# Kernel optimization log

Hardware: AMD Instinct MI355X
Metric: run time of the kernel (lower is better)

## Reference

```python
import jax, jax.numpy as jnp
import numpy as np

N_NODES = 100000
N_REL = 4
N_EDGES = 400000
IN_F, H_F, OUT_F = 128, 128, 64


def setup_inputs() -> dict:
    key = jax.random.key(0)
    ks = jax.random.split(key, 7)
    x = jax.random.normal(ks[0], (N_NODES, IN_F), dtype=jnp.float32)
    src_idx = jax.random.randint(ks[1], (N_REL, N_EDGES), 0, N_NODES, dtype=jnp.int64)
    dst_idx = jax.random.randint(ks[2], (N_REL, N_EDGES), 0, N_NODES, dtype=jnp.int64)
    # Glorot-ish scale for the per-relation GraphConv weights
    W1 = jax.random.normal(ks[3], (N_REL, IN_F, H_F), dtype=jnp.float32) * (1.0 / np.sqrt(IN_F))
    b1 = jnp.zeros((N_REL, H_F), dtype=jnp.float32)
    W2 = jax.random.normal(ks[4], (N_REL, H_F, OUT_F), dtype=jnp.float32) * (1.0 / np.sqrt(H_F))
    b2 = jnp.zeros((N_REL, OUT_F), dtype=jnp.float32)
    return {"x": x, "src_idx": src_idx, "dst_idx": dst_idx,
            "W1": W1, "b1": b1, "W2": W2, "b2": b2}


def _graph_conv(x, src, dst, W, b):
    """DGL GraphConv with norm='both': out = D_in^{-1/2} A^T D_out^{-1/2} x W + b."""
    n = x.shape[0]
    ones = jnp.ones(src.shape[0], dtype=x.dtype)
    deg_out = jnp.maximum(jax.ops.segment_sum(ones, src, num_segments=n), 1.0)
    deg_in = jnp.maximum(jax.ops.segment_sum(ones, dst, num_segments=n), 1.0)
    xn = x * jax.lax.rsqrt(deg_out)[:, None]              # [N, F] src-side norm
    msg = jnp.take(xn, src, axis=0)                        # [E, F] gather
    agg = jax.ops.segment_sum(msg, dst, num_segments=n)   # [N, F] scatter-add
    agg = agg * jax.lax.rsqrt(deg_in)[:, None]            # dst-side norm
    return agg @ W + b


def _hetero_layer(x, src_idx, dst_idx, Ws, bs):
    # per-relation conv, sum-aggregated across relations (HeteroGraphConv 'sum')
    per_rel = jax.vmap(lambda s, d, W, b: _graph_conv(x, s, d, W, b))(src_idx, dst_idx, Ws, bs)
    return per_rel.sum(axis=0)


def reference(x, src_idx, dst_idx, W1, b1, W2, b2):
    h = jax.nn.relu(_hetero_layer(x, src_idx, dst_idx, W1, b1))
    return _hetero_layer(h, src_idx, dst_idx, W2, b2)
```

## Files before the change

### kernel.cpp

```cpp
#include <hip/hip_runtime.h>
#include <hip/hip_bf16.h>

#define NN 100000
#define NR 4
#define NE 400000
#define INF 128
#define HF 128
#define OUTF 64

#define WIN 16384
#define WIN2 (WIN / 2)
#define NWIN 7
#define SUB 16
#define SLICE (NE / SUB)

#define GB 782
#define CB 1563
#define CSRB (NR * CB)
#define PADB 391
#define FGRID (GB + CSRB + PADB)

typedef __attribute__((ext_vector_type(8))) short s16x8;
typedef __attribute__((ext_vector_type(4))) float f32x4;

__global__ __launch_bounds__(256) void deg_win_kernel(const int* __restrict__ src,
                                                      const int* __restrict__ dst,
                                                      unsigned int* __restrict__ parts) {
    __shared__ unsigned int hist[WIN2];
    int arr = blockIdx.z;
    int r   = blockIdx.y;
    int win = blockIdx.x / SUB;
    int sub = blockIdx.x % SUB;
    const int4* idx4 = (const int4*)((arr ? dst : src) + (size_t)r * NE + (size_t)sub * SLICE);
    int base = win * WIN;

    uint4 z4 = make_uint4(0, 0, 0, 0);
    for (int i = threadIdx.x; i < WIN2 / 4; i += 256) ((uint4*)hist)[i] = z4;
    __syncthreads();

    auto proc = [&](int4 v) {
        int a;
        a = v.x - base; if ((unsigned)a < WIN) atomicAdd(&hist[a >> 1], 1u << ((a & 1) << 4));
        a = v.y - base; if ((unsigned)a < WIN) atomicAdd(&hist[a >> 1], 1u << ((a & 1) << 4));
        a = v.z - base; if ((unsigned)a < WIN) atomicAdd(&hist[a >> 1], 1u << ((a & 1) << 4));
        a = v.w - base; if ((unsigned)a < WIN) atomicAdd(&hist[a >> 1], 1u << ((a & 1) << 4));
    };

    constexpr int NV = SLICE / 4;
    int i = threadIdx.x;
    for (; i + 256 < NV; i += 512) {
        int4 va = idx4[i];
        int4 vb = idx4[i + 256];
        proc(va);
        proc(vb);
    }
    if (i < NV) proc(idx4[i]);
    __syncthreads();

    unsigned int* outp = parts + ((((size_t)arr * NR + r) * NWIN + win) * SUB + sub) * WIN2;
    for (int j = threadIdx.x; j < WIN2 / 4; j += 256)
        ((uint4*)outp)[j] = ((const uint4*)hist)[j];
}

__global__ void red_norm_kernel(const unsigned int* __restrict__ parts, int* __restrict__ deg_tot,
                                float* __restrict__ rno, float* __restrict__ rni) {
    int n = blockIdx.x * blockDim.x + threadIdx.x;
    if (n >= NN) return;
    if (n == 0) deg_tot[NN] = 0;
    int win = n / WIN, off = n % WIN;
    int word = off >> 1, sh = (off & 1) << 4;
    int tot = 0;
    #pragma unroll
    for (int r = 0; r < NR; r++) {
        const unsigned int* p0 = parts + (((size_t)0 * NR + r) * NWIN + win) * SUB * WIN2 + word;
        const unsigned int* p1 = parts + (((size_t)1 * NR + r) * NWIN + win) * SUB * WIN2 + word;
        int so = 0, si = 0;
        #pragma unroll
        for (int s = 0; s < SUB; s++) {
            so += (p0[(size_t)s * WIN2] >> sh) & 0xFFFFu;
            si += (p1[(size_t)s * WIN2] >> sh) & 0xFFFFu;
        }
        rno[(size_t)r * NN + n] = rsqrtf(fmaxf((float)so, 1.0f));
        rni[(size_t)r * NN + n] = rsqrtf(fmaxf((float)si, 1.0f));
        tot += si;
    }
    deg_tot[n] = tot;
}

__global__ void scan_block_kernel(const int* __restrict__ in, int* __restrict__ out,
                                  int* __restrict__ blockSums, int n) {
    __shared__ int sd[256];
    int t = threadIdx.x;
    int base = blockIdx.x * 1024 + t * 4;
    int v[4];
    #pragma unroll
    for (int j = 0; j < 4; j++) v[j] = (base + j < n) ? ((in[base + j] + 7) & ~7) : 0;
    int ts = v[0] + v[1] + v[2] + v[3];
    sd[t] = ts;
    __syncthreads();
    int acc = ts;
    for (int off = 1; off < 256; off <<= 1) {
        int x = (t >= off) ? sd[t - off] : 0;
        __syncthreads();
        acc += x; sd[t] = acc;
        __syncthreads();
    }
    int run = acc - ts;
    #pragma unroll
    for (int j = 0; j < 4; j++) {
        if (base + j < n) out[base + j] = run;
        run += v[j];
    }
    if (t == 255) blockSums[blockIdx.x] = acc;
}

__global__ void scan_sums_kernel(int* __restrict__ blockSums, int nb) {
    __shared__ int sd[512];
    int t = threadIdx.x;
    int v = (t < nb) ? blockSums[t] : 0;
    sd[t] = v;
    __syncthreads();
    int acc = v;
    for (int off = 1; off < 512; off <<= 1) {
        int x = (t >= off) ? sd[t - off] : 0;
        __syncthreads();
        acc += x; sd[t] = acc;
        __syncthreads();
    }
    if (t < nb) blockSums[t] = acc - v;
}

__global__ void scan_add_kernel(int* __restrict__ row_ptr, const int* __restrict__ blockSums,
                                int* __restrict__ cursor, int n) {
    int i = blockIdx.x * blockDim.x + threadIdx.x;
    if (i < n) {
        int v = row_ptr[i] + blockSums[i >> 10];
        row_ptr[i] = v;
        if (i < NN) cursor[i] = v;
    }
}

__global__ void prep_kernel(const float* __restrict__ W1, const float* __restrict__ W2,
                            const float* __restrict__ b1, const float* __restrict__ b2,
                            __hip_bfloat16* __restrict__ Wt1, __hip_bfloat16* __restrict__ Wt2,
                            float* __restrict__ bsum1, float* __restrict__ bsum2) {
    if (blockIdx.x == 384) {
        int t = threadIdx.x;
        if (t < HF) {
            float s = 0.f;
            for (int r = 0; r < NR; r++) s += b1[r * HF + t];
            bsum1[t] = s;
        } else if (t < HF + OUTF) {
            int f = t - HF;
            float s = 0.f;
            for (int r = 0; r < NR; r++) s += b2[r * OUTF + f];
            bsum2[f] = s;
        }
        return;
    }
    int id = blockIdx.x * 256 + threadIdx.x;
    if (id < NR * HF * INF) {
        int r = id >> 14, rem = id & 16383;
        int n_ = rem >> 7, k = rem & 127;
        Wt1[id] = __float2bfloat16(W1[((size_t)r * INF + k) * HF + n_]);
    } else {
        int id2 = id - NR * HF * INF;
        if (id2 < NR * OUTF * HF) {
            int r = id2 >> 13, rem = id2 & 8191;
            int n_ = rem >> 7, k = rem & 127;
            Wt2[id2] = __float2bfloat16(W2[((size_t)r * HF + k) * OUTF + n_]);
        }
    }
}

__device__ __forceinline__ s16x8 pack_bf16x8(float4 a0, float4 a1) {
    union { s16x8 v; __hip_bfloat162 h[4]; } u;
    u.h[0] = __float22bfloat162_rn(make_float2(a0.x, a0.y));
    u.h[1] = __float22bfloat162_rn(make_float2(a0.z, a0.w));
    u.h[2] = __float22bfloat162_rn(make_float2(a1.x, a1.y));
    u.h[3] = __float22bfloat162_rn(make_float2(a1.z, a1.w));
    return u.v;
}

__device__ __forceinline__ void load_lds_16(const void* g, void* l) {
    __builtin_amdgcn_global_load_lds(
        (const __attribute__((address_space(1))) void*)g,
        (__attribute__((address_space(3))) void*)l, 16, 0, 0);
}

template<int F, typename AT>
__device__ __forceinline__ void gemm_body(int mbase, const AT* __restrict__ Xb,
                                          const __hip_bfloat16* __restrict__ Wt,
                                          __hip_bfloat16* __restrict__ Zb, int nrel,
                                          __hip_bfloat16* Bs) {
    constexpr int NT = F / 16;
    constexpr int NG = F * 16;

    int tid  = threadIdx.x;
    int wid  = tid >> 6;
    int lane = tid & 63;
    int quad = lane >> 4;
    int l16  = lane & 15;
    int sw   = l16 & 7;

    int bofs[4];
    #pragma unroll
    for (int kb = 0; kb < 4; kb++)
        bofs[kb] = l16 * 256 + (((kb * 4 + quad) ^ sw) << 4);

    s16x8 afr[2][4];
    #pragma unroll
    for (int mt = 0; mt < 2; mt++) {
        int mrow = mbase + mt * 64 + wid * 16 + l16;
        if (mrow >= NN) mrow = NN - 1;
        #pragma unroll
        for (int kb = 0; kb < 4; kb++) {
            if constexpr (sizeof(AT) == 4) {
                const float* xr = (const float*)Xb + (size_t)mrow * 128 + kb * 32 + quad * 8;
                float4 a0 = *(const float4*)xr;
                float4 a1 = *(const float4*)(xr + 4);
                afr[mt][kb] = pack_bf16x8(a0, a1);
            } else {
                afr[mt][kb] = *(const s16x8*)((const __hip_bfloat16*)Xb + (size_t)mrow * 128 + kb * 32 + quad * 8);
            }
        }
    }

    for (int rel = 0; rel < nrel; rel++) {
        if (rel) __syncthreads();

        {
            const char* W = (const char*)(Wt + (size_t)rel * F * 128);
            #pragma unroll
            for (int it = 0; it < NG / 256; it++) {
                int dg = it * 256 + tid;
                int sg = dg ^ ((dg >> 4) & 7);
                load_lds_16(W + (size_t)sg * 16, (char*)Bs + (size_t)(dg & ~63) * 16);
            }
        }
        __syncthreads();

        __hip_bfloat16* Z = Zb + (size_t)rel * NN * F;

        f32x4 acc[2][NT];
        #pragma unroll
        for (int nt = 0; nt < NT; nt++) {
            acc[0][nt] = (f32x4){0.f, 0.f, 0.f, 0.f};
            acc[1][nt] = (f32x4){0.f, 0.f, 0.f, 0.f};
            #pragma unroll
            for (int kb = 0; kb < 4; kb++) {
                s16x8 bfr = *(const s16x8*)((const char*)Bs + nt * 4096 + bofs[kb]);
                acc[0][nt] = __builtin_amdgcn_mfma_f32_16x16x32_bf16(bfr, afr[0][kb], acc[0][nt], 0, 0, 0);
                acc[1][nt] = __builtin_amdgcn_mfma_f32_16x16x32_bf16(bfr, afr[1][kb], acc[1][nt], 0, 0, 0);
            }
        }

        #pragma unroll
        for (int mt = 0; mt < 2; mt++) {
            int g = mbase + mt * 64 + wid * 16 + l16;
            if (g < NN) {
                #pragma unroll
                for (int nt = 0; nt < NT; nt++) {
                    union { uint2 u; __hip_bfloat162 h[2]; } o;
                    o.h[0] = __float22bfloat162_rn(make_float2(acc[mt][nt][0], acc[mt][nt][1]));
                    o.h[1] = __float22bfloat162_rn(make_float2(acc[mt][nt][2], acc[mt][nt][3]));
                    *(uint2*)(Z + (size_t)g * F + nt * 16 + quad * 4) = o.u;
                }
            }
        }
    }
}

__global__ __launch_bounds__(256, 3) void fused1_kernel(
        const float* __restrict__ x, const __hip_bfloat16* __restrict__ Wt1,
        __hip_bfloat16* __restrict__ Zb,
        const int* __restrict__ src, const int* __restrict__ dst,
        const float* __restrict__ rno, const float* __restrict__ rni,
        int* __restrict__ cursor, int2* __restrict__ edges,
        const int* __restrict__ row_ptr, const int* __restrict__ deg_tot) {
    __shared__ __attribute__((aligned(16))) __hip_bfloat16 Bs[HF * 128];
    int b = blockIdx.x;
    bool isg = (b % 3 == 1) && (b / 3 < GB);
    if (isg) {
        gemm_body<HF, float>((b / 3) * 128, x, Wt1, Zb, NR, Bs);
        return;
    }
    int cnt = (b <= 1) ? 0 : ((b + 1) / 3);
    if (cnt > GB) cnt = GB;
    int ng = b - cnt;
    if (ng < CSRB) {
        int r = ng / CB;
        int i = (ng % CB) * 256 + threadIdx.x;
        if (i < NE) {
            int s = src[(size_t)r * NE + i];
            int d = dst[(size_t)r * NE + i];
            int pos = atomicAdd(&cursor[d], 1);
            float c = rno[(size_t)r * NN + s] * rni[(size_t)r * NN + d];
            edges[pos] = make_int2((r * NN + s) << 8, __float_as_int(c));
        }
    } else {
        int n = (ng - CSRB) * 256 + threadIdx.x;
        if (n < NN) {
            int pb = row_ptr[n] + deg_tot[n];
            int pe = row_ptr[n + 1];
            for (int i = pb; i < pe; i++) edges[i] = make_int2(0, 0);
        }
    }
}

template<int F, typename AT>
__global__ __launch_bounds__(256, 3) void gemm_all(const AT* __restrict__ Xb,
                                                   const __hip_bfloat16* __restrict__ Wt,
                                                   __hip_bfloat16* __restrict__ Zb, int nrel) {
    __shared__ __attribute__((aligned(16))) __hip_bfloat16 Bs[F * 128];
    gemm_body<F, AT>(blockIdx.x * 128, Xb, Wt, Zb, nrel, Bs);
}

template<int F, bool RELU, bool OUT_F32>
__global__ __launch_bounds__(256) void gather_merged(const int* __restrict__ row_ptr,
                              const int2* __restrict__ edges,
                              const __hip_bfloat16* __restrict__ Zb,
                              float* __restrict__ outf, __hip_bfloat16* __restrict__ outb,
                              const float* __restrict__ bsum) {
    int wid  = threadIdx.x >> 6;
    int lane = threadIdx.x & 63;
    int n = blockIdx.x * 4 + wid;
    int beg = row_ptr[n];
    int end = row_ptr[n + 1];

    if constexpr (F == 128) {
        const char* Zl = (const char*)Zb + lane * 4;
        float2 a = *(const float2*)(bsum + lane * 2);
        for (int p = beg; p < end; p += 8) {
            int2 e[8];
            #pragma unroll
            for (int j = 0; j < 8; j++) e[j] = edges[p + j];
            float2 zz[8];
            #pragma unroll
            for (int j = 0; j < 8; j++)
                zz[j] = __bfloat1622float2(*(const __hip_bfloat162*)(Zl + e[j].x));
            #pragma unroll
            for (int j = 0; j < 8; j++) {
                float c = __int_as_float(e[j].y);
                a.x = fmaf(c, zz[j].x, a.x);
                a.y = fmaf(c, zz[j].y, a.y);
            }
        }
        if constexpr (RELU) { a.x = fmaxf(a.x, 0.f); a.y = fmaxf(a.y, 0.f); }
        *(__hip_bfloat162*)(outb + (size_t)n * 128 + lane * 2) = __float22bfloat162_rn(a);
    } else {
        const char* Zl = (const char*)Zb + lane * 2;
        float a = bsum[lane];
        for (int p = beg; p < end; p += 8) {
            int2 e[8];
            #pragma unroll
            for (int j = 0; j < 8; j++) e[j] = edges[p + j];
            float zz[8];
            #pragma unroll
            for (int j = 0; j < 8; j++)
                zz[j] = __bfloat162float(*(const __hip_bfloat16*)(Zl + (e[j].x >> 1)));
            #pragma unroll
            for (int j = 0; j < 8; j++) a = fmaf(__int_as_float(e[j].y), zz[j], a);
        }
        if constexpr (RELU) a = fmaxf(a, 0.f);
        if constexpr (OUT_F32) outf[(size_t)n * 64 + lane] = a;
        else outb[(size_t)n * 64 + lane] = __float2bfloat16(a);
    }
}

extern "C" void kernel_launch(void* const* d_in, const int* in_sizes, int n_in,
                              void* d_out, int out_size, void* d_ws, size_t ws_size,
                              hipStream_t stream) {
    const float* x   = (const float*)d_in[0];
    const int*   src = (const int*)  d_in[1];
    const int*   dst = (const int*)  d_in[2];
    const float* W1  = (const float*)d_in[3];
    const float* b1  = (const float*)d_in[4];
    const float* W2  = (const float*)d_in[5];
    const float* b2  = (const float*)d_in[6];
    float* out = (float*)d_out;

    constexpr int RN = NR * NN;
    constexpr int NSC = NN + 1;
    constexpr int NB = (NSC + 1023) / 1024;

    char* p = (char*)d_ws;
    int*   deg_tot   = (int*)p;   p += ((size_t)NN + 16) * 4;
    float* rno       = (float*)p; p += (size_t)RN * 4;
    float* rni       = (float*)p; p += (size_t)RN * 4;
    int*   row_ptr   = (int*)p;   p += ((size_t)NN + 16) * 4;
    int*   cursor    = (int*)p;   p += (size_t)NN * 4;
    int*   blockSums = (int*)p;   p += 1024 * 4;
    int2*  edges     = (int2*)p;  p += ((size_t)NR * NE + 8 * NN) * 8;
    float* bsum1 = (float*)p; p += HF * 4;
    float* bsum2 = (float*)p; p += OUTF * 4;
    __hip_bfloat16* hb  = (__hip_bfloat16*)p; p += (size_t)NN * HF * 2;
    __hip_bfloat16* Wt1 = (__hip_bfloat16*)p; p += (size_t)NR * HF * INF * 2;
    __hip_bfloat16* Wt2 = (__hip_bfloat16*)p; p += (size_t)NR * OUTF * HF * 2;
    __hip_bfloat16* Zb = (__hip_bfloat16*)p;
    unsigned int* parts = (unsigned int*)Zb;

    prep_kernel<<<385, 256, 0, stream>>>(W1, W2, b1, b2, Wt1, Wt2, bsum1, bsum2);
    deg_win_kernel<<<dim3(NWIN * SUB, NR, 2), 256, 0, stream>>>(src, dst, parts);
    red_norm_kernel<<<(NN + 255) / 256, 256, 0, stream>>>(parts, deg_tot, rno, rni);
    scan_block_kernel<<<NB, 256, 0, stream>>>(deg_tot, row_ptr, blockSums, NSC);
    scan_sums_kernel<<<1, 512, 0, stream>>>(blockSums, NB);
    scan_add_kernel<<<(NSC + 255) / 256, 256, 0, stream>>>(row_ptr, blockSums, cursor, NSC);

    fused1_kernel<<<FGRID, 256, 0, stream>>>(x, Wt1, Zb, src, dst, rno, rni,
                                             cursor, edges, row_ptr, deg_tot);

    constexpr int GG = NN / 4;

    gather_merged<HF, true, false><<<GG, 256, 0, stream>>>(
        row_ptr, edges, Zb, nullptr, hb, bsum1);

    gemm_all<OUTF, __hip_bfloat16><<<GB, 256, 0, stream>>>(hb, Wt2, Zb, 4);
    gather_merged<OUTF, false, true><<<GG, 256, 0, stream>>>(
        row_ptr, edges, Zb, out, nullptr, bsum2);
}
```

Measured before the change: 367.9 us.

## Replace per-node atomic CSR scatter with two-pass bucketed edge sort

Per-destination global atomics in the edge scatter are replaced by a two-pass sort. The first pass bins edges into 256 destination buckets, staging them in LDS and flushing them in chunks to a temp buffer, and runs interleaved with the first-layer GEMM blocks. A second kernel then sorts each bucket by destination in shared memory, writes it out with coalesced stores and zero-fills the padding. The aim is to cut scattered global atomics and random 8-byte writes, at the cost of an extra kernel launch, a temp buffer that aliases hb, and a slower fallback path when a bucket overflows LDS.

After: 418.9 us. +13.9%, slower.

```diff
diff --git a/kernel.cpp b/kernel.cpp
--- a/kernel.cpp
+++ b/kernel.cpp
@@ -15,10 +15,12 @@
 #define SLICE (NE / SUB)
 
 #define GB 782
-#define CB 1563
-#define CSRB (NR * CB)
-#define PADB 391
-#define FGRID (GB + CSRB + PADB)
+#define P1B 256
+#define FGRID (GB + P1B)
+
+#define NBKT 256
+#define BKTW 391
+#define CAP2 12288
 
 typedef __attribute__((ext_vector_type(8))) short s16x8;
 typedef __attribute__((ext_vector_type(4))) float f32x4;
@@ -131,12 +133,12 @@
 }
 
 __global__ void scan_add_kernel(int* __restrict__ row_ptr, const int* __restrict__ blockSums,
-                                int* __restrict__ cursor, int n) {
+                                int* __restrict__ bcur, int n) {
     int i = blockIdx.x * blockDim.x + threadIdx.x;
     if (i < n) {
         int v = row_ptr[i] + blockSums[i >> 10];
         row_ptr[i] = v;
-        if (i < NN) cursor[i] = v;
+        if (i < NN && (i % BKTW) == 0) bcur[i / BKTW] = v;
     }
 }
 
@@ -271,39 +273,104 @@
     }
 }
 
-__global__ __launch_bounds__(256, 3) void fused1_kernel(
+__global__ __launch_bounds__(256, 3) void fusedA_kernel(
         const float* __restrict__ x, const __hip_bfloat16* __restrict__ Wt1,
         __hip_bfloat16* __restrict__ Zb,
         const int* __restrict__ src, const int* __restrict__ dst,
         const float* __restrict__ rno, const float* __restrict__ rni,
-        int* __restrict__ cursor, int2* __restrict__ edges,
-        const int* __restrict__ row_ptr, const int* __restrict__ deg_tot) {
-    __shared__ __attribute__((aligned(16))) __hip_bfloat16 Bs[HF * 128];
+        int* __restrict__ bcur, int2* __restrict__ temp) {
+    __shared__ __attribute__((aligned(16))) char sm[NBKT * 16 * 8 + NBKT * 4];
     int b = blockIdx.x;
-    bool isg = (b % 3 == 1) && (b / 3 < GB);
-    if (isg) {
-        gemm_body<HF, float>((b / 3) * 128, x, Wt1, Zb, NR, Bs);
+    bool isp = ((b & 3) == 3) && ((b >> 2) < P1B);
+    if (!isp) {
+        int cnt = (b + 1) >> 2; if (cnt > P1B) cnt = P1B;
+        gemm_body<HF, float>((b - cnt) * 128, x, Wt1, Zb, NR, (__hip_bfloat16*)sm);
         return;
     }
-    int cnt = (b <= 1) ? 0 : ((b + 1) / 3);
-    if (cnt > GB) cnt = GB;
-    int ng = b - cnt;
-    if (ng < CSRB) {
-        int r = ng / CB;
-        int i = (ng % CB) * 256 + threadIdx.x;
-        if (i < NE) {
-            int s = src[(size_t)r * NE + i];
-            int d = dst[(size_t)r * NE + i];
-            int pos = atomicAdd(&cursor[d], 1);
+    int2 (*lbuf)[16] = (int2(*)[16])sm;
+    int* lcur = (int*)(sm + NBKT * 16 * 8);
+    int blk = b >> 2;
+    int r   = blk >> 6;
+    int i0  = (blk & 63) * 6250;
+    int tid = threadIdx.x;
+    lcur[tid] = 0;
+    __syncthreads();
+    for (int e0 = 0; e0 < 6250; e0 += 256) {
+        int e = e0 + tid;
+        if (e < 6250) {
+            int s = src[(size_t)r * NE + i0 + e];
+            int d = dst[(size_t)r * NE + i0 + e];
+            unsigned k = (unsigned)d / BKTW;
+            int dlo = d - (int)k * BKTW;
             float c = rno[(size_t)r * NN + s] * rni[(size_t)r * NN + d];
-            edges[pos] = make_int2((r * NN + s) << 8, __float_as_int(c));
-        }
+            int2 rec = make_int2(((r * NN + s) << 9) | dlo, __float_as_int(c));
+            int pos = atomicAdd(&lcur[k], 1);
+            if (pos < 16) lbuf[k][pos] = rec;
+            else {
+                int g = atomicAdd(&bcur[k], 1);
+                temp[g] = rec;
+            }
+        }
+        __syncthreads();
+        int fill = lcur[tid]; if (fill > 16) fill = 16;
+        int nout = fill & ~7;
+        if (nout) {
+            int g = atomicAdd(&bcur[tid], nout);
+            int2* dq = temp + g;
+            for (int j = 0; j < nout; j++) dq[j] = lbuf[tid][j];
+            int rem = fill - nout;
+            for (int j = 0; j < rem; j++) lbuf[tid][j] = lbuf[tid][nout + j];
+            lcur[tid] = rem;
+        } else lcur[tid] = fill;
+        __syncthreads();
+    }
+    int fill = lcur[tid]; if (fill > 16) fill = 16;
+    if (fill) {
+        int g = atomicAdd(&bcur[tid], fill);
+        for (int j = 0; j < fill; j++) temp[g + j] = lbuf[tid][j];
+    }
+}
+
+__global__ __launch_bounds__(256) void pass2_kernel(const int* __restrict__ bcur,
+                                                    const int2* __restrict__ temp,
+                                                    const int* __restrict__ row_ptr,
+                                                    int2* __restrict__ edges) {
+    __shared__ __attribute__((aligned(16))) int2 stg[CAP2];
+    __shared__ int cur[BKTW + 1];
+    int k   = blockIdx.x;
+    int D0  = k * BKTW;
+    int ND  = NN - D0; if (ND > BKTW) ND = BKTW;
+    int base = row_ptr[D0];
+    int span = row_ptr[D0 + ND] - base;
+    int cnt  = bcur[k] - base;
+    int tid  = threadIdx.x;
+
+    if (span <= CAP2) {
+        int4 z = make_int4(0, 0, 0, 0);
+        for (int j = tid; j < (span >> 1); j += 256) ((int4*)stg)[j] = z;
+        for (int i = tid; i < ND; i += 256) cur[i] = row_ptr[D0 + i] - base;
+        __syncthreads();
+        for (int j = tid; j < cnt; j += 256) {
+            int2 rec = temp[base + j];
+            int i = rec.x & 511;
+            int p = atomicAdd(&cur[i], 1);
+            stg[p] = make_int2((rec.x >> 9) << 8, rec.y);
+        }
+        __syncthreads();
+        int4* dq = (int4*)(edges + base);
+        const int4* sq = (const int4*)stg;
+        for (int j = tid; j < (span >> 1); j += 256) dq[j] = sq[j];
     } else {
-        int n = (ng - CSRB) * 256 + threadIdx.x;
-        if (n < NN) {
-            int pb = row_ptr[n] + deg_tot[n];
-            int pe = row_ptr[n + 1];
-            for (int i = pb; i < pe; i++) edges[i] = make_int2(0, 0);
+        int4 z = make_int4(0, 0, 0, 0);
+        int4* dq = (int4*)(edges + base);
+        for (int j = tid; j < (span >> 1); j += 256) dq[j] = z;
+        for (int i = tid; i < ND; i += 256) cur[i] = row_ptr[D0 + i];
+        __syncthreads();
+        for (int j = tid; j < cnt; j += 256) {
+            int2 rec = temp[base + j];
+            int i = rec.x & 511;
+            int p = atomicAdd(&cur[i], 1);
+            edges[p] = make_int2((rec.x >> 9) << 8, rec.y);
         }
     }
 }
@@ -399,16 +466,19 @@
     __hip_bfloat16* Wt2 = (__hip_bfloat16*)p; p += (size_t)NR * OUTF * HF * 2;
     __hip_bfloat16* Zb = (__hip_bfloat16*)p;
     unsigned int* parts = (unsigned int*)Zb;
+    int* bcur = blockSums + 512;
+    int2* temp = (int2*)hb;
 
     prep_kernel<<<385, 256, 0, stream>>>(W1, W2, b1, b2, Wt1, Wt2, bsum1, bsum2);
     deg_win_kernel<<<dim3(NWIN * SUB, NR, 2), 256, 0, stream>>>(src, dst, parts);
     red_norm_kernel<<<(NN + 255) / 256, 256, 0, stream>>>(parts, deg_tot, rno, rni);
     scan_block_kernel<<<NB, 256, 0, stream>>>(deg_tot, row_ptr, blockSums, NSC);
     scan_sums_kernel<<<1, 512, 0, stream>>>(blockSums, NB);
-    scan_add_kernel<<<(NSC + 255) / 256, 256, 0, stream>>>(row_ptr, blockSums, cursor, NSC);
-
-    fused1_kernel<<<FGRID, 256, 0, stream>>>(x, Wt1, Zb, src, dst, rno, rni,
-                                             cursor, edges, row_ptr, deg_tot);
+    scan_add_kernel<<<(NSC + 255) / 256, 256, 0, stream>>>(row_ptr, blockSums, bcur, NSC);
+
+    fusedA_kernel<<<FGRID, 256, 0, stream>>>(x, Wt1, Zb, src, dst, rno, rni, bcur, temp);
+
+    pass2_kernel<<<NBKT, 256, 0, stream>>>(bcur, temp, row_ptr, edges);
 
     constexpr int GG = NN / 4;
 
```
